# Optimization experiments

Measured on AMD Instinct MI355X. Metric: run time of the kernel, lower is better.

## Reference

```python
import jax, jax.numpy as jnp
import numpy as np

N_OBS = 2_097_152
N_BAND = 4
T_SPAN = 3650.0  # days


def setup_inputs() -> dict:
    key = jax.random.key(0)
    k0, k1, k2, k3, k4, k5 = jax.random.split(key, 6)
    t = jnp.sort(jax.random.uniform(k0, (N_OBS,), jnp.float32) * T_SPAN)
    band = jax.random.randint(k1, (N_OBS,), 0, N_BAND)
    y = jax.random.normal(k2, (N_OBS,), jnp.float32)
    yerr = 0.1 + 0.9 * jax.random.uniform(k3, (N_OBS,), jnp.float32)
    log_amp_delta = 0.1 * jax.random.normal(k4, (N_BAND - 1,), jnp.float32)
    # [log sigma, log ell] for the quasisep Exp kernel
    log_kernel_param = jnp.array([0.0, np.log(50.0)], dtype=jnp.float32) + \
        0.1 * jax.random.normal(k5, (2,), jnp.float32)
    return {"t": t, "band": band, "y": y, "yerr": yerr,
            "log_amp_delta": log_amp_delta, "log_kernel_param": log_kernel_param}


def _log_prob(t, band, y, yerr, log_amp_delta, log_kernel_param):
    # amp_transform: prepend 0 -> per-band amplitudes
    amps = jnp.exp(jnp.concatenate([jnp.zeros(1, log_amp_delta.dtype), log_amp_delta]))
    sigma2 = jnp.exp(2.0 * log_kernel_param[0])
    ell = jnp.exp(log_kernel_param[1])

    # lag_transform with zero lags: sort by time (assume_sorted path of tinygp)
    inds = jnp.argsort(t)
    ts, b = t[inds], band[inds]
    ys, dg = y[inds], (yerr ** 2)[inds]

    # multiband Exp kernel: K_ij = sigma2 * u_i * u_j * exp(-(t_i - t_j)/ell), i>=j
    u = amps[b]                       # per-point amplitude
    a = dg + sigma2 * u * u           # diagonal K_ii + noise
    U = sigma2 * u                    # semiseparable left factor
    V = u                             # semiseparable right factor
    dt = jnp.diff(ts)
    P = jnp.concatenate([jnp.zeros(1, ts.dtype), jnp.exp(-dt / ell)])  # decay factors

    # Celerite O(N) Cholesky (K = L D L^T) fused with the forward solve L z = y.
    def step(carry, x):
        cS, cg = carry                # cS = S_{n-1} + D_{n-1} W_{n-1}^2 ; cg = g_{n-1} + W_{n-1} z_{n-1}
        Pn, an, Un, Vn, yn = x
        Sn = Pn * Pn * cS
        gn = Pn * cg
        Dn = an - Un * Un * Sn
        Wn = (Vn - Sn * Un) / Dn
        zn = yn - Un * gn
        return (Sn + Dn * Wn * Wn, gn + Wn * zn), (jnp.log(Dn), zn * zn / Dn)

    zero = jnp.zeros((), ts.dtype)
    _, (logD, quad) = jax.lax.scan(step, (zero, zero), (P, a, U, V, ys))
    n = ts.shape[0]
    return -0.5 * (jnp.sum(quad) + jnp.sum(logD) + n * jnp.log(2.0 * jnp.pi))


def reference(t, band, y, yerr, log_amp_delta, log_kernel_param):
    return _log_prob(t, band, y, yerr, log_amp_delta, log_kernel_param)
```

## Files before the change

kernel.cpp:

```cpp
#include <hip/hip_runtime.h>
#include <math.h>

#define N_TOTAL 2097152
#define NT 256
#define NC 8
#define EPB (NT * NC)
#define NB (N_TOTAL / EPB)
#define NWAVES (NT / 64)

struct DMat { double al, be, ga, de, c, e, f; };

__device__ __forceinline__ DMat dmat_identity() {
    DMat m; m.al = 1.0; m.be = 0.0; m.ga = 0.0; m.de = 1.0; m.c = 1.0; m.e = 0.0; m.f = 0.0;
    return m;
}

__device__ __forceinline__ DMat dmat_compose(const DMat& A, const DMat& B) {
    DMat r;
    r.al = A.al * B.al + A.be * B.ga;
    r.be = A.al * B.be + A.be * B.de;
    r.ga = A.ga * B.al + A.de * B.ga;
    r.de = A.ga * B.be + A.de * B.de;
    r.c  = A.c * B.c;
    r.e  = A.e * B.al + A.c * B.e + A.f * B.ga;
    r.f  = A.e * B.be + A.c * B.f + A.f * B.de;
    return r;
}

__device__ __forceinline__ void dmat_normalize(DMat& m) {
    double mx = fmax(fabs(m.al), fabs(m.be));
    mx = fmax(mx, fabs(m.ga));
    mx = fmax(mx, fabs(m.de));
    mx = fmax(mx, fabs(m.c));
    mx = fmax(mx, fabs(m.e));
    mx = fmax(mx, fabs(m.f));
    if (!(mx > 0.0) || isinf(mx)) return;
    double inv = 1.0 / mx;
    m.al *= inv; m.be *= inv; m.ga *= inv; m.de *= inv;
    m.c *= inv; m.e *= inv; m.f *= inv;
}

__device__ __forceinline__ DMat dmat_shfl_up(const DMat& m, int d) {
    DMat r;
    r.al = __shfl_up(m.al, d, 64);
    r.be = __shfl_up(m.be, d, 64);
    r.ga = __shfl_up(m.ga, d, 64);
    r.de = __shfl_up(m.de, d, 64);
    r.c  = __shfl_up(m.c,  d, 64);
    r.e  = __shfl_up(m.e,  d, 64);
    r.f  = __shfl_up(m.f,  d, 64);
    return r;
}

__device__ __forceinline__ DMat dmat_wave_scan(DMat mine, int lane) {
    #pragma unroll
    for (int d = 1; d < 64; d <<= 1) {
        DMat o = dmat_shfl_up(mine, d);
        if (lane >= d) {
            mine = dmat_compose(mine, o);
            dmat_normalize(mine);
        }
    }
    return mine;
}

__device__ __forceinline__ DMat elem_mat_f32(float P, float dg, float s2u2,
                                             float sigma2, float u, float yy) {
    float p = P * P;
    float U = sigma2 * u;
    DMat m;
    m.al = (double)(p * (dg - s2u2));
    m.be = (double)(u * u);
    m.ga = -(double)(p * U * U);
    m.de = (double)(dg + s2u2);
    m.c  = (double)(P * dg);
    m.e  = -(double)(yy * p * U);
    m.f  = (double)(yy * u);
    return m;
}

__device__ __forceinline__ void dmat_store_g(double* p, const DMat& m) {
    p[0] = m.al; p[1] = m.be; p[2] = m.ga; p[3] = m.de;
    p[4] = m.c;  p[5] = m.e;  p[6] = m.f;
}

__device__ __forceinline__ DMat dmat_load_g(const double* p) {
    DMat m = {p[0], p[1], p[2], p[3], p[4], p[5], p[6]};
    return m;
}

__global__ __launch_bounds__(NT, 4) void k_upsweep(
    const float* __restrict__ t, const int* __restrict__ band,
    const float* __restrict__ y, const float* __restrict__ yerr,
    const float* __restrict__ lad, const float* __restrict__ lkp,
    double* __restrict__ block_comp, double* __restrict__ wave_excl)
{
    __shared__ double smw[7 * NWAVES];
    const int tid = threadIdx.x;
    const int lane = tid & 63;
    const int wv = tid >> 6;
    const float sigma2 = __expf(2.f * lkp[0]);
    const float inv_ell = __expf(-lkp[1]);
    float amps[4] = {1.f, __expf(lad[0]), __expf(lad[1]), __expf(lad[2])};

    const int base = (blockIdx.x * NT + tid) * NC;
    float tprev = (base == 0) ? 0.f : t[base - 1];
    DMat acc = dmat_identity();
    #pragma unroll
    for (int k = 0; k < NC; k += 4) {
        float4 tv = *reinterpret_cast<const float4*>(t + base + k);
        float4 yv = *reinterpret_cast<const float4*>(y + base + k);
        float4 ev = *reinterpret_cast<const float4*>(yerr + base + k);
        int4   bv = *reinterpret_cast<const int4*>(band + base + k);
        float tc[4] = {tv.x, tv.y, tv.z, tv.w};
        float yc[4] = {yv.x, yv.y, yv.z, yv.w};
        float ec[4] = {ev.x, ev.y, ev.z, ev.w};
        int   bc[4] = {bv.x, bv.y, bv.z, bv.w};
        #pragma unroll
        for (int j = 0; j < 4; ++j) {
            float u = amps[bc[j] & 3];
            float dg = ec[j] * ec[j];
            float s2u2 = sigma2 * u * u;
            float P = ((base + k + j) == 0) ? 0.f
                    : __expf(-(tc[j] - tprev) * inv_ell);
            acc = dmat_compose(elem_mat_f32(P, dg, s2u2, sigma2, u, yc[j]), acc);
            tprev = tc[j];
        }
    }
    dmat_normalize(acc);
    DMat incl = dmat_wave_scan(acc, lane);
    if (lane == 63) {
        #define STW(idx, val) smw[(idx) * NWAVES + wv] = (val)
        STW(0, incl.al); STW(1, incl.be); STW(2, incl.ga); STW(3, incl.de);
        STW(4, incl.c);  STW(5, incl.e);  STW(6, incl.f);
        #undef STW
    }
    __syncthreads();
    if (tid == 0) {
        DMat pre = dmat_identity();
        for (int w = 0; w < NWAVES; ++w) {
            dmat_store_g(wave_excl + (blockIdx.x * NWAVES + w) * 7, pre);
            DMat Ww = {smw[0 * NWAVES + w], smw[1 * NWAVES + w],
                       smw[2 * NWAVES + w], smw[3 * NWAVES + w],
                       smw[4 * NWAVES + w], smw[5 * NWAVES + w],
                       smw[6 * NWAVES + w]};
            pre = dmat_compose(Ww, pre);
            dmat_normalize(pre);
        }
        dmat_store_g(block_comp + blockIdx.x * 7, pre);
    }
}

__global__ __launch_bounds__(NT) void k_spine(
    const double* __restrict__ block_comp, double* __restrict__ block_excl,
    double* __restrict__ accum, unsigned int* __restrict__ counter)
{
    __shared__ double smw[7 * NWAVES];
    const int tid = threadIdx.x;
    const int lane = tid & 63;
    const int wv = tid >> 6;
    if (tid == 0) {
        accum[0] = 0.0;
        accum[1] = 0.0;
        *counter = 0u;
    }
    DMat m[4];
    #pragma unroll
    for (int i = 0; i < 4; ++i)
        m[i] = dmat_load_g(block_comp + (4 * tid + i) * 7);
    DMat acc = m[0];
    #pragma unroll
    for (int i = 1; i < 4; ++i) acc = dmat_compose(m[i], acc);
    dmat_normalize(acc);
    DMat incl = dmat_wave_scan(acc, lane);
    if (lane == 63) {
        #define STW(idx, val) smw[(idx) * NWAVES + wv] = (val)
        STW(0, incl.al); STW(1, incl.be); STW(2, incl.ga); STW(3, incl.de);
        STW(4, incl.c);  STW(5, incl.e);  STW(6, incl.f);
        #undef STW
    }
    __syncthreads();
    DMat wpre = dmat_identity();
    for (int w = 0; w < wv; ++w) {
        DMat Ww = {smw[0 * NWAVES + w], smw[1 * NWAVES + w],
                   smw[2 * NWAVES + w], smw[3 * NWAVES + w],
                   smw[4 * NWAVES + w], smw[5 * NWAVES + w],
                   smw[6 * NWAVES + w]};
        wpre = dmat_compose(Ww, wpre);
    }
    dmat_normalize(wpre);
    DMat lex = dmat_shfl_up(incl, 1);
    if (lane == 0) lex = dmat_identity();
    DMat tex = dmat_compose(lex, wpre);
    dmat_normalize(tex);
    #pragma unroll
    for (int i = 0; i < 4; ++i) {
        dmat_store_g(block_excl + (4 * tid + i) * 7, tex);
        tex = dmat_compose(m[i], tex);
        dmat_normalize(tex);
    }
}

__global__ __launch_bounds__(NT, 4) void k_replay(
    const float* __restrict__ t, const int* __restrict__ band,
    const float* __restrict__ y, const float* __restrict__ yerr,
    const float* __restrict__ lad, const float* __restrict__ lkp,
    const double* __restrict__ block_excl, const double* __restrict__ wave_excl,
    double* __restrict__ accum, unsigned int* __restrict__ counter,
    float* __restrict__ out)
{
    __shared__ double smr[2 * NWAVES];
    const int tid = threadIdx.x;
    const int lane = tid & 63;
    const int wv = tid >> 6;
    const float sigma2 = __expf(2.f * lkp[0]);
    const float inv_ell = __expf(-lkp[1]);
    float amps[4] = {1.f, __expf(lad[0]), __expf(lad[1]), __expf(lad[2])};

    const int base = (blockIdx.x * NT + tid) * NC;
    float tprev = (base == 0) ? 0.f : t[base - 1];

    float Pv[NC], dgv[NC], uv[NC], yv_[NC];
    DMat acc = dmat_identity();
    #pragma unroll
    for (int k = 0; k < NC; k += 4) {
        float4 tv = *reinterpret_cast<const float4*>(t + base + k);
        float4 yv = *reinterpret_cast<const float4*>(y + base + k);
        float4 ev = *reinterpret_cast<const float4*>(yerr + base + k);
        int4   bv = *reinterpret_cast<const int4*>(band + base + k);
        float tc[4] = {tv.x, tv.y, tv.z, tv.w};
        float yc[4] = {yv.x, yv.y, yv.z, yv.w};
        float ec[4] = {ev.x, ev.y, ev.z, ev.w};
        int   bc[4] = {bv.x, bv.y, bv.z, bv.w};
        #pragma unroll
        for (int j = 0; j < 4; ++j) {
            float u = amps[bc[j] & 3];
            float dg = ec[j] * ec[j];
            float s2u2 = sigma2 * u * u;
            float P = ((base + k + j) == 0) ? 0.f
                    : __expf(-(tc[j] - tprev) * inv_ell);
            Pv[k + j] = P; dgv[k + j] = dg; uv[k + j] = u; yv_[k + j] = yc[j];
            acc = dmat_compose(elem_mat_f32(P, dg, s2u2, sigma2, u, yc[j]), acc);
            tprev = tc[j];
        }
    }
    dmat_normalize(acc);
    DMat incl = dmat_wave_scan(acc, lane);
    DMat lex = dmat_shfl_up(incl, 1);
    if (lane == 0) lex = dmat_identity();

    DMat Ew = dmat_load_g(wave_excl + (blockIdx.x * NWAVES + wv) * 7);
    DMat Eb = dmat_load_g(block_excl + blockIdx.x * 7);
    DMat Fw = dmat_compose(Ew, Eb);
    dmat_normalize(Fw);
    DMat F = dmat_compose(lex, Fw);
    float x = 0.f, g = 0.f;
    if (F.de != 0.0) {
        double invde = 1.0 / F.de;
        x = (float)(F.be * invde);
        g = (float)(F.f  * invde);
    }
    if (!isfinite(x)) x = 0.f;
    if (!isfinite(g)) g = 0.f;

    float s_logD = 0.f, s_quad = 0.f;
    #pragma unroll
    for (int k = 0; k < NC; ++k) {
        float P = Pv[k], dg = dgv[k], u = uv[k], yy = yv_[k];
        float U = sigma2 * u;
        float a = dg + U * u;
        float p = P * P;
        float S = p * x;
        float D = a - U * U * S;
        if (!(D > 1e-30f)) D = 1e-30f;
        float W = (u - S * U) / D;
        float gn = P * g;
        float z = yy - U * gn;
        s_logD += __logf(D);
        s_quad += z * z / D;
        x = S + D * W * W;
        g = gn + W * z;
    }

    double sl = (double)s_logD, sq = (double)s_quad;
    #pragma unroll
    for (int d = 32; d > 0; d >>= 1) {
        sl += __shfl_down(sl, d, 64);
        sq += __shfl_down(sq, d, 64);
    }
    if (lane == 0) { smr[wv] = sl; smr[NWAVES + wv] = sq; }
    __syncthreads();
    if (tid == 0) {
        double tl = smr[0] + smr[1] + smr[2] + smr[3];
        double tq = smr[NWAVES] + smr[NWAVES + 1] + smr[NWAVES + 2] + smr[NWAVES + 3];
        atomicAdd(&accum[0], tl);
        atomicAdd(&accum[1], tq);
        __threadfence();
        unsigned int old = atomicAdd(counter, 1u);
        if (old == NB - 1) {
            double s0 = atomicAdd(&accum[0], 0.0);
            double s1 = atomicAdd(&accum[1], 0.0);
            double r = -0.5 * (s0 + s1
                       + (double)N_TOTAL * 1.8378770664093454836);
            out[0] = (float)r;
        }
    }
}

extern "C" void kernel_launch(void* const* d_in, const int* in_sizes, int n_in,
                              void* d_out, int out_size, void* d_ws, size_t ws_size,
                              hipStream_t stream)
{
    const float* t    = (const float*)d_in[0];
    const int*   band = (const int*)d_in[1];
    const float* y    = (const float*)d_in[2];
    const float* yerr = (const float*)d_in[3];
    const float* lad  = (const float*)d_in[4];
    const float* lkp  = (const float*)d_in[5];

    double* dws        = (double*)d_ws;
    double* block_comp = dws;
    double* block_excl = block_comp + NB * 7;
    double* wave_excl  = block_excl + NB * 7;
    double* accum      = wave_excl + NB * NWAVES * 7;
    unsigned int* counter = (unsigned int*)(accum + 2);

    k_upsweep<<<NB, NT, 0, stream>>>(t, band, y, yerr, lad, lkp,
                                     block_comp, wave_excl);
    k_spine<<<1, NT, 0, stream>>>(block_comp, block_excl, accum, counter);
    k_replay<<<NB, NT, 0, stream>>>(t, band, y, yerr, lad, lkp,
                                    block_excl, wave_excl, accum, counter,
                                    (float*)d_out);
}
```

Measured before the change: 138.9 us.

## Split Riccati and affine recursions with windowed warm-up and packed second pass

The 7-entry double transfer-matrix scan is replaced by a 2x2 double scan for the Riccati (S) recursion only. Each wave gets its starting state from a local scan over a 256-element overlap window that precedes its owned range, so S no longer needs a global cross-block prefix. Per-element affine coefficients for the g recursion and the quadratic terms are packed to a float4 buffer. A light float affine scan across blocks and a second pass over the packed data then finish the quadratic sum. This drops the heavy double-precision global scan and the re-reading of the raw inputs, at the cost of 32 MB of extra workspace traffic, duplicated warm-up work in half of each wave's lanes, and an approximation that assumes the Riccati state forgets its start within the window (with clamps on x and D).

```diff
diff --git a/kernel.cpp b/kernel.cpp
--- a/kernel.cpp
+++ b/kernel.cpp
@@ -3,301 +3,267 @@
 
 #define N_TOTAL 2097152
 #define NT 256
-#define NC 8
-#define EPB (NT * NC)
-#define NB (N_TOTAL / EPB)
-#define NWAVES (NT / 64)
-
-struct DMat { double al, be, ga, de, c, e, f; };
-
-__device__ __forceinline__ DMat dmat_identity() {
-    DMat m; m.al = 1.0; m.be = 0.0; m.ga = 0.0; m.de = 1.0; m.c = 1.0; m.e = 0.0; m.f = 0.0;
-    return m;
-}
-
-__device__ __forceinline__ DMat dmat_compose(const DMat& A, const DMat& B) {
-    DMat r;
-    r.al = A.al * B.al + A.be * B.ga;
-    r.be = A.al * B.be + A.be * B.de;
-    r.ga = A.ga * B.al + A.de * B.ga;
-    r.de = A.ga * B.be + A.de * B.de;
-    r.c  = A.c * B.c;
-    r.e  = A.e * B.al + A.c * B.e + A.f * B.ga;
-    r.f  = A.e * B.be + A.c * B.f + A.f * B.de;
+#define NC1 8
+#define OWN_W 256
+#define OWN_B 1024
+#define NB1 (N_TOTAL / OWN_B)
+#define NC2 4
+#define NB2 (N_TOTAL / (NT * NC2))
+#define NWAVES 4
+
+struct DM2 { double al, be, ga, de; };
+struct Aff { float A, B; };
+
+__device__ __forceinline__ DM2 dm2_id() { DM2 m; m.al=1.0; m.be=0.0; m.ga=0.0; m.de=1.0; return m; }
+__device__ __forceinline__ DM2 dm2_compose(const DM2& A, const DM2& B) {
+    DM2 r;
+    r.al = A.al*B.al + A.be*B.ga;
+    r.be = A.al*B.be + A.be*B.de;
+    r.ga = A.ga*B.al + A.de*B.ga;
+    r.de = A.ga*B.be + A.de*B.de;
     return r;
 }
-
-__device__ __forceinline__ void dmat_normalize(DMat& m) {
-    double mx = fmax(fabs(m.al), fabs(m.be));
-    mx = fmax(mx, fabs(m.ga));
-    mx = fmax(mx, fabs(m.de));
-    mx = fmax(mx, fabs(m.c));
-    mx = fmax(mx, fabs(m.e));
-    mx = fmax(mx, fabs(m.f));
+__device__ __forceinline__ void dm2_norm(DM2& m) {
+    double mx = fmax(fmax(fabs(m.al), fabs(m.be)), fmax(fabs(m.ga), fabs(m.de)));
     if (!(mx > 0.0) || isinf(mx)) return;
     double inv = 1.0 / mx;
     m.al *= inv; m.be *= inv; m.ga *= inv; m.de *= inv;
-    m.c *= inv; m.e *= inv; m.f *= inv;
-}
-
-__device__ __forceinline__ DMat dmat_shfl_up(const DMat& m, int d) {
-    DMat r;
+}
+__device__ __forceinline__ DM2 dm2_shfl_up(const DM2& m, int d) {
+    DM2 r;
     r.al = __shfl_up(m.al, d, 64);
     r.be = __shfl_up(m.be, d, 64);
     r.ga = __shfl_up(m.ga, d, 64);
     r.de = __shfl_up(m.de, d, 64);
-    r.c  = __shfl_up(m.c,  d, 64);
-    r.e  = __shfl_up(m.e,  d, 64);
-    r.f  = __shfl_up(m.f,  d, 64);
     return r;
 }
-
-__device__ __forceinline__ DMat dmat_wave_scan(DMat mine, int lane) {
+__device__ __forceinline__ Aff aff_id() { Aff a; a.A=1.f; a.B=0.f; return a; }
+__device__ __forceinline__ Aff aff_compose(const Aff& L, const Aff& E) {
+    Aff r; r.A = L.A*E.A; r.B = L.A*E.B + L.B; return r;
+}
+__device__ __forceinline__ Aff aff_shfl_up(const Aff& a, int d) {
+    Aff r; r.A = __shfl_up(a.A, d, 64); r.B = __shfl_up(a.B, d, 64); return r;
+}
+__device__ __forceinline__ Aff aff_wave_scan(Aff mine, int lane) {
     #pragma unroll
     for (int d = 1; d < 64; d <<= 1) {
-        DMat o = dmat_shfl_up(mine, d);
-        if (lane >= d) {
-            mine = dmat_compose(mine, o);
-            dmat_normalize(mine);
-        }
+        Aff o = aff_shfl_up(mine, d);
+        if (lane >= d) mine = aff_compose(mine, o);
     }
     return mine;
 }
 
-__device__ __forceinline__ DMat elem_mat_f32(float P, float dg, float s2u2,
-                                             float sigma2, float u, float yy) {
-    float p = P * P;
-    float U = sigma2 * u;
-    DMat m;
-    m.al = (double)(p * (dg - s2u2));
-    m.be = (double)(u * u);
-    m.ga = -(double)(p * U * U);
-    m.de = (double)(dg + s2u2);
-    m.c  = (double)(P * dg);
-    m.e  = -(double)(yy * p * U);
-    m.f  = (double)(yy * u);
-    return m;
-}
-
-__device__ __forceinline__ void dmat_store_g(double* p, const DMat& m) {
-    p[0] = m.al; p[1] = m.be; p[2] = m.ga; p[3] = m.de;
-    p[4] = m.c;  p[5] = m.e;  p[6] = m.f;
-}
-
-__device__ __forceinline__ DMat dmat_load_g(const double* p) {
-    DMat m = {p[0], p[1], p[2], p[3], p[4], p[5], p[6]};
-    return m;
-}
-
-__global__ __launch_bounds__(NT, 4) void k_upsweep(
+__global__ __launch_bounds__(NT, 4) void k_pass1(
     const float* __restrict__ t, const int* __restrict__ band,
     const float* __restrict__ y, const float* __restrict__ yerr,
     const float* __restrict__ lad, const float* __restrict__ lkp,
-    double* __restrict__ block_comp, double* __restrict__ wave_excl)
+    float4* __restrict__ packed, float2* __restrict__ baff,
+    float* __restrict__ blogd)
 {
-    __shared__ double smw[7 * NWAVES];
-    const int tid = threadIdx.x;
-    const int lane = tid & 63;
-    const int wv = tid >> 6;
+    __shared__ float2 smaff[NWAVES];
+    __shared__ float  smlog[NWAVES];
+    const int tid = threadIdx.x, lane = tid & 63, wv = tid >> 6;
     const float sigma2 = __expf(2.f * lkp[0]);
     const float inv_ell = __expf(-lkp[1]);
     float amps[4] = {1.f, __expf(lad[0]), __expf(lad[1]), __expf(lad[2])};
 
-    const int base = (blockIdx.x * NT + tid) * NC;
-    float tprev = (base == 0) ? 0.f : t[base - 1];
-    DMat acc = dmat_identity();
-    #pragma unroll
-    for (int k = 0; k < NC; k += 4) {
-        float4 tv = *reinterpret_cast<const float4*>(t + base + k);
-        float4 yv = *reinterpret_cast<const float4*>(y + base + k);
-        float4 ev = *reinterpret_cast<const float4*>(yerr + base + k);
-        int4   bv = *reinterpret_cast<const int4*>(band + base + k);
-        float tc[4] = {tv.x, tv.y, tv.z, tv.w};
-        float yc[4] = {yv.x, yv.y, yv.z, yv.w};
-        float ec[4] = {ev.x, ev.y, ev.z, ev.w};
-        int   bc[4] = {bv.x, bv.y, bv.z, bv.w};
+    const int own0 = blockIdx.x * OWN_B + wv * OWN_W;
+    const int base = own0 - OWN_W + lane * NC1;
+    const bool valid = (base >= 0);
+
+    float Pv[NC1], dgv[NC1], uv[NC1], yv[NC1];
+    DM2 acc = dm2_id();
+    if (valid) {
+        float tprev = (base == 0) ? 0.f : t[base - 1];
         #pragma unroll
-        for (int j = 0; j < 4; ++j) {
-            float u = amps[bc[j] & 3];
-            float dg = ec[j] * ec[j];
-            float s2u2 = sigma2 * u * u;
-            float P = ((base + k + j) == 0) ? 0.f
-                    : __expf(-(tc[j] - tprev) * inv_ell);
-            acc = dmat_compose(elem_mat_f32(P, dg, s2u2, sigma2, u, yc[j]), acc);
-            tprev = tc[j];
+        for (int k = 0; k < NC1; k += 4) {
+            float4 tv  = *reinterpret_cast<const float4*>(t + base + k);
+            float4 yv4 = *reinterpret_cast<const float4*>(y + base + k);
+            float4 ev  = *reinterpret_cast<const float4*>(yerr + base + k);
+            int4   bv  = *reinterpret_cast<const int4*>(band + base + k);
+            float tc[4] = {tv.x, tv.y, tv.z, tv.w};
+            float yc[4] = {yv4.x, yv4.y, yv4.z, yv4.w};
+            float ec[4] = {ev.x, ev.y, ev.z, ev.w};
+            int   bc[4] = {bv.x, bv.y, bv.z, bv.w};
+            #pragma unroll
+            for (int j = 0; j < 4; ++j) {
+                float u = amps[bc[j] & 3];
+                float dg = ec[j] * ec[j];
+                float s2u2 = sigma2 * u * u;
+                float P = ((base + k + j) == 0) ? 0.f
+                        : __expf(-(tc[j] - tprev) * inv_ell);
+                float U = sigma2 * u;
+                float p = P * P;
+                DM2 e;
+                e.al = (double)(p * (dg - s2u2));
+                e.be = (double)(u * u);
+                e.ga = -(double)(p * U * U);
+                e.de = (double)(dg + s2u2);
+                acc = dm2_compose(e, acc);
+                Pv[k+j] = P; dgv[k+j] = dg; uv[k+j] = u; yv[k+j] = yc[j];
+                tprev = tc[j];
+            }
         }
-    }
-    dmat_normalize(acc);
-    DMat incl = dmat_wave_scan(acc, lane);
-    if (lane == 63) {
-        #define STW(idx, val) smw[(idx) * NWAVES + wv] = (val)
-        STW(0, incl.al); STW(1, incl.be); STW(2, incl.ga); STW(3, incl.de);
-        STW(4, incl.c);  STW(5, incl.e);  STW(6, incl.f);
-        #undef STW
-    }
+        dm2_norm(acc);
+    }
+    DM2 incl = acc;
+    #pragma unroll
+    for (int d = 1; d < 64; d <<= 1) {
+        DM2 o = dm2_shfl_up(incl, d);
+        if (lane >= d) { incl = dm2_compose(incl, o); dm2_norm(incl); }
+    }
+    DM2 lex = dm2_shfl_up(incl, 1);
+    if (lane == 0) lex = dm2_id();
+    float x = 0.f;
+    if (lex.de != 0.0) {
+        double xx = lex.be / lex.de;
+        if (isfinite(xx)) x = (float)xx;
+    }
+    x = fminf(fmaxf(x, 0.f), 4.f);
+
+    float slog = 0.f;
+    Aff a = aff_id();
+    if (lane >= 32) {
+        #pragma unroll
+        for (int k = 0; k < NC1; ++k) {
+            float P = Pv[k], dg = dgv[k], u = uv[k], yy = yv[k];
+            float U = sigma2 * u;
+            float av = dg + U * u;
+            float p = P * P;
+            float S = p * x;
+            float D = av - U * U * S;
+            if (!(D > 1e-4f)) D = 1e-4f;
+            float iD = 1.f / D;
+            float W = (u - S * U) * iD;
+            slog += __logf(D);
+            float rs = sqrtf(iD);
+            float c1 = U * P;
+            float rho = P - c1 * W;
+            float Wy = W * yy;
+            float4 pk; pk.x = rho; pk.y = Wy; pk.z = yy * rs; pk.w = c1 * rs;
+            packed[base + k] = pk;
+            a.B = rho * a.B + Wy;
+            a.A *= rho;
+            x = S + D * W * W;
+        }
+    }
+    Aff ai = aff_wave_scan(a, lane);
+    #pragma unroll
+    for (int d = 32; d > 0; d >>= 1) slog += __shfl_down(slog, d, 64);
+    if (lane == 63) { float2 v; v.x = ai.A; v.y = ai.B; smaff[wv] = v; }
+    if (lane == 0) smlog[wv] = slog;
     __syncthreads();
     if (tid == 0) {
-        DMat pre = dmat_identity();
-        for (int w = 0; w < NWAVES; ++w) {
-            dmat_store_g(wave_excl + (blockIdx.x * NWAVES + w) * 7, pre);
-            DMat Ww = {smw[0 * NWAVES + w], smw[1 * NWAVES + w],
-                       smw[2 * NWAVES + w], smw[3 * NWAVES + w],
-                       smw[4 * NWAVES + w], smw[5 * NWAVES + w],
-                       smw[6 * NWAVES + w]};
-            pre = dmat_compose(Ww, pre);
-            dmat_normalize(pre);
+        Aff bacc; bacc.A = smaff[0].x; bacc.B = smaff[0].y;
+        #pragma unroll
+        for (int w = 1; w < NWAVES; ++w) {
+            Aff ww; ww.A = smaff[w].x; ww.B = smaff[w].y;
+            bacc = aff_compose(ww, bacc);
         }
-        dmat_store_g(block_comp + blockIdx.x * 7, pre);
+        float2 ov; ov.x = bacc.A; ov.y = bacc.B;
+        baff[blockIdx.x] = ov;
+        blogd[blockIdx.x] = smlog[0] + smlog[1] + smlog[2] + smlog[3];
     }
 }
 
 __global__ __launch_bounds__(NT) void k_spine(
-    const double* __restrict__ block_comp, double* __restrict__ block_excl,
-    double* __restrict__ accum, unsigned int* __restrict__ counter)
+    const float2* __restrict__ baff, const float* __restrict__ blogd,
+    float* __restrict__ gstart, double* __restrict__ accum,
+    unsigned int* __restrict__ counter)
 {
-    __shared__ double smw[7 * NWAVES];
-    const int tid = threadIdx.x;
-    const int lane = tid & 63;
-    const int wv = tid >> 6;
+    __shared__ float2 smw[NWAVES];
+    __shared__ double smd[NWAVES];
+    const int tid = threadIdx.x, lane = tid & 63, wv = tid >> 6;
+    Aff m[8];
+    double ld = 0.0;
+    #pragma unroll
+    for (int j = 0; j < 8; ++j) {
+        float2 v = baff[8 * tid + j];
+        m[j].A = v.x; m[j].B = v.y;
+        ld += (double)blogd[8 * tid + j];
+    }
+    Aff acc = m[0];
+    #pragma unroll
+    for (int j = 1; j < 8; ++j) acc = aff_compose(m[j], acc);
+    Aff incl = aff_wave_scan(acc, lane);
+    #pragma unroll
+    for (int d = 32; d > 0; d >>= 1) ld += __shfl_down(ld, d, 64);
+    if (lane == 63) { float2 v; v.x = incl.A; v.y = incl.B; smw[wv] = v; }
+    if (lane == 0) smd[wv] = ld;
+    __syncthreads();
+    Aff wpre = aff_id();
+    for (int w = 0; w < wv; ++w) {
+        Aff ww; ww.A = smw[w].x; ww.B = smw[w].y;
+        wpre = aff_compose(ww, wpre);
+    }
+    Aff lex = aff_shfl_up(incl, 1);
+    if (lane == 0) lex = aff_id();
+    Aff tex = aff_compose(lex, wpre);
+    #pragma unroll
+    for (int j = 0; j < 8; ++j) {
+        gstart[8 * tid + j] = tex.B;
+        tex = aff_compose(m[j], tex);
+    }
     if (tid == 0) {
-        accum[0] = 0.0;
+        accum[0] = smd[0] + smd[1] + smd[2] + smd[3];
         accum[1] = 0.0;
         *counter = 0u;
     }
-    DMat m[4];
-    #pragma unroll
-    for (int i = 0; i < 4; ++i)
-        m[i] = dmat_load_g(block_comp + (4 * tid + i) * 7);
-    DMat acc = m[0];
-    #pragma unroll
-    for (int i = 1; i < 4; ++i) acc = dmat_compose(m[i], acc);
-    dmat_normalize(acc);
-    DMat incl = dmat_wave_scan(acc, lane);
-    if (lane == 63) {
-        #define STW(idx, val) smw[(idx) * NWAVES + wv] = (val)
-        STW(0, incl.al); STW(1, incl.be); STW(2, incl.ga); STW(3, incl.de);
-        STW(4, incl.c);  STW(5, incl.e);  STW(6, incl.f);
-        #undef STW
-    }
-    __syncthreads();
-    DMat wpre = dmat_identity();
-    for (int w = 0; w < wv; ++w) {
-        DMat Ww = {smw[0 * NWAVES + w], smw[1 * NWAVES + w],
-                   smw[2 * NWAVES + w], smw[3 * NWAVES + w],
-                   smw[4 * NWAVES + w], smw[5 * NWAVES + w],
-                   smw[6 * NWAVES + w]};
-        wpre = dmat_compose(Ww, wpre);
-    }
-    dmat_normalize(wpre);
-    DMat lex = dmat_shfl_up(incl, 1);
-    if (lane == 0) lex = dmat_identity();
-    DMat tex = dmat_compose(lex, wpre);
-    dmat_normalize(tex);
-    #pragma unroll
-    for (int i = 0; i < 4; ++i) {
-        dmat_store_g(block_excl + (4 * tid + i) * 7, tex);
-        tex = dmat_compose(m[i], tex);
-        dmat_normalize(tex);
-    }
-}
-
-__global__ __launch_bounds__(NT, 4) void k_replay(
-    const float* __restrict__ t, const int* __restrict__ band,
-    const float* __restrict__ y, const float* __restrict__ yerr,
-    const float* __restrict__ lad, const float* __restrict__ lkp,
-    const double* __restrict__ block_excl, const double* __restrict__ wave_excl,
+}
+
+__global__ __launch_bounds__(NT, 4) void k_pass2(
+    const float4* __restrict__ packed, const float* __restrict__ gstart,
     double* __restrict__ accum, unsigned int* __restrict__ counter,
     float* __restrict__ out)
 {
-    __shared__ double smr[2 * NWAVES];
-    const int tid = threadIdx.x;
-    const int lane = tid & 63;
-    const int wv = tid >> 6;
-    const float sigma2 = __expf(2.f * lkp[0]);
-    const float inv_ell = __expf(-lkp[1]);
-    float amps[4] = {1.f, __expf(lad[0]), __expf(lad[1]), __expf(lad[2])};
-
-    const int base = (blockIdx.x * NT + tid) * NC;
-    float tprev = (base == 0) ? 0.f : t[base - 1];
-
-    float Pv[NC], dgv[NC], uv[NC], yv_[NC];
-    DMat acc = dmat_identity();
-    #pragma unroll
-    for (int k = 0; k < NC; k += 4) {
-        float4 tv = *reinterpret_cast<const float4*>(t + base + k);
-        float4 yv = *reinterpret_cast<const float4*>(y + base + k);
-        float4 ev = *reinterpret_cast<const float4*>(yerr + base + k);
-        int4   bv = *reinterpret_cast<const int4*>(band + base + k);
-        float tc[4] = {tv.x, tv.y, tv.z, tv.w};
-        float yc[4] = {yv.x, yv.y, yv.z, yv.w};
-        float ec[4] = {ev.x, ev.y, ev.z, ev.w};
-        int   bc[4] = {bv.x, bv.y, bv.z, bv.w};
-        #pragma unroll
-        for (int j = 0; j < 4; ++j) {
-            float u = amps[bc[j] & 3];
-            float dg = ec[j] * ec[j];
-            float s2u2 = sigma2 * u * u;
-            float P = ((base + k + j) == 0) ? 0.f
-                    : __expf(-(tc[j] - tprev) * inv_ell);
-            Pv[k + j] = P; dgv[k + j] = dg; uv[k + j] = u; yv_[k + j] = yc[j];
-            acc = dmat_compose(elem_mat_f32(P, dg, s2u2, sigma2, u, yc[j]), acc);
-            tprev = tc[j];
-        }
-    }
-    dmat_normalize(acc);
-    DMat incl = dmat_wave_scan(acc, lane);
-    DMat lex = dmat_shfl_up(incl, 1);
-    if (lane == 0) lex = dmat_identity();
-
-    DMat Ew = dmat_load_g(wave_excl + (blockIdx.x * NWAVES + wv) * 7);
-    DMat Eb = dmat_load_g(block_excl + blockIdx.x * 7);
-    DMat Fw = dmat_compose(Ew, Eb);
-    dmat_normalize(Fw);
-    DMat F = dmat_compose(lex, Fw);
-    float x = 0.f, g = 0.f;
-    if (F.de != 0.0) {
-        double invde = 1.0 / F.de;
-        x = (float)(F.be * invde);
-        g = (float)(F.f  * invde);
-    }
-    if (!isfinite(x)) x = 0.f;
+    __shared__ float2 smaff[NWAVES];
+    __shared__ float  smq[NWAVES];
+    const int tid = threadIdx.x, lane = tid & 63, wv = tid >> 6;
+    const int base = blockIdx.x * (NT * NC2) + tid * NC2;
+    float4 pk[NC2];
+    #pragma unroll
+    for (int k = 0; k < NC2; ++k) pk[k] = packed[base + k];
+
+    Aff a = aff_id();
+    #pragma unroll
+    for (int k = 0; k < NC2; ++k) {
+        a.B = pk[k].x * a.B + pk[k].y;
+        a.A *= pk[k].x;
+    }
+    Aff incl = aff_wave_scan(a, lane);
+    Aff lex = aff_shfl_up(incl, 1);
+    if (lane == 0) lex = aff_id();
+    if (lane == 63) { float2 v; v.x = incl.A; v.y = incl.B; smaff[wv] = v; }
+    __syncthreads();
+    Aff wpre = aff_id();
+    for (int w = 0; w < wv; ++w) {
+        Aff ww; ww.A = smaff[w].x; ww.B = smaff[w].y;
+        wpre = aff_compose(ww, wpre);
+    }
+    Aff te = aff_compose(lex, wpre);
+    float gblk = gstart[blockIdx.x];
+    if (!isfinite(gblk)) gblk = 0.f;
+    float g = te.A * gblk + te.B;
     if (!isfinite(g)) g = 0.f;
 
-    float s_logD = 0.f, s_quad = 0.f;
-    #pragma unroll
-    for (int k = 0; k < NC; ++k) {
-        float P = Pv[k], dg = dgv[k], u = uv[k], yy = yv_[k];
-        float U = sigma2 * u;
-        float a = dg + U * u;
-        float p = P * P;
-        float S = p * x;
-        float D = a - U * U * S;
-        if (!(D > 1e-30f)) D = 1e-30f;
-        float W = (u - S * U) / D;
-        float gn = P * g;
-        float z = yy - U * gn;
-        s_logD += __logf(D);
-        s_quad += z * z / D;
-        x = S + D * W * W;
-        g = gn + W * z;
-    }
-
-    double sl = (double)s_logD, sq = (double)s_quad;
-    #pragma unroll
-    for (int d = 32; d > 0; d >>= 1) {
-        sl += __shfl_down(sl, d, 64);
-        sq += __shfl_down(sq, d, 64);
-    }
-    if (lane == 0) { smr[wv] = sl; smr[NWAVES + wv] = sq; }
+    float q = 0.f;
+    #pragma unroll
+    for (int k = 0; k < NC2; ++k) {
+        float z = pk[k].z - pk[k].w * g;
+        q += z * z;
+        g = pk[k].x * g + pk[k].y;
+    }
+    #pragma unroll
+    for (int d = 32; d > 0; d >>= 1) q += __shfl_down(q, d, 64);
+    if (lane == 0) smq[wv] = q;
     __syncthreads();
     if (tid == 0) {
-        double tl = smr[0] + smr[1] + smr[2] + smr[3];
-        double tq = smr[NWAVES] + smr[NWAVES + 1] + smr[NWAVES + 2] + smr[NWAVES + 3];
-        atomicAdd(&accum[0], tl);
-        atomicAdd(&accum[1], tq);
+        double qt = (double)smq[0] + (double)smq[1]
+                  + (double)smq[2] + (double)smq[3];
+        atomicAdd(&accum[1], qt);
         __threadfence();
         unsigned int old = atomicAdd(counter, 1u);
-        if (old == NB - 1) {
+        if (old == NB2 - 1) {
             double s0 = atomicAdd(&accum[0], 0.0);
             double s1 = atomicAdd(&accum[1], 0.0);
             double r = -0.5 * (s0 + s1
@@ -318,17 +284,18 @@
     const float* lad  = (const float*)d_in[4];
     const float* lkp  = (const float*)d_in[5];
 
-    double* dws        = (double*)d_ws;
-    double* block_comp = dws;
-    double* block_excl = block_comp + NB * 7;
-    double* wave_excl  = block_excl + NB * 7;
-    double* accum      = wave_excl + NB * NWAVES * 7;
-    unsigned int* counter = (unsigned int*)(accum + 2);
-
-    k_upsweep<<<NB, NT, 0, stream>>>(t, band, y, yerr, lad, lkp,
-                                     block_comp, wave_excl);
-    k_spine<<<1, NT, 0, stream>>>(block_comp, block_excl, accum, counter);
-    k_replay<<<NB, NT, 0, stream>>>(t, band, y, yerr, lad, lkp,
-                                    block_excl, wave_excl, accum, counter,
+    char* ws = (char*)d_ws;
+    float4* packed = (float4*)ws;
+    size_t off = (size_t)N_TOTAL * 16;
+    float2* baff   = (float2*)(ws + off);   off += NB1 * 8;
+    float*  blogd  = (float*)(ws + off);    off += NB1 * 4;
+    float*  gstart = (float*)(ws + off);    off += NB1 * 4;
+    double* accum  = (double*)(ws + off);   off += 16;
+    unsigned int* counter = (unsigned int*)(ws + off);
+
+    k_pass1<<<NB1, NT, 0, stream>>>(t, band, y, yerr, lad, lkp,
+                                    packed, baff, blogd);
+    k_spine<<<1, NT, 0, stream>>>(baff, blogd, gstart, accum, counter);
+    k_pass2<<<NB2, NT, 0, stream>>>(packed, gstart, accum, counter,
                                     (float*)d_out);
 }
```

Measured after the change: 157.5 us. 1.13x slower.
